# Optimization experiments

Hardware: AMD Instinct MI355X
Metric: run time of the kernel (lower is better)

## Reference

```python
import jax, jax.numpy as jnp
import numpy as np

I_DIM = 20000        # item (node) count; emb_mat has I_DIM+1 rows
EMB_DIM = 128        # input embedding dim
D_DIM = 128          # hidden (scaled) dim
N_EDGES = 640000     # number of (src, dst) edges


def setup_inputs() -> dict:
    key = jax.random.key(0)
    k1, k2, k3, k4 = jax.random.split(key, 4)
    emb_mat = jax.random.normal(k1, (I_DIM + 1, EMB_DIM), dtype=jnp.float32)
    # edges must be sorted by source node (column 0) so that the original
    # tf.repeat(segment_sums, bincount(src)) trick is well-defined.
    edge = jax.random.randint(k2, (N_EDGES, 2), 0, I_DIM + 1, dtype=jnp.int64)
    order = jnp.argsort(edge[:, 0])
    edge = edge[order]
    W_scale = jax.random.normal(k3, (EMB_DIM, D_DIM), dtype=jnp.float32) * 0.05
    b_scale = jnp.zeros((D_DIM,), dtype=jnp.float32)
    W_att = jax.random.normal(k4, (2 * D_DIM, 1), dtype=jnp.float32) * 0.05
    b_att = jnp.zeros((1,), dtype=jnp.float32)
    return {"emb_mat": emb_mat, "edge": edge, "W_scale": W_scale,
            "b_scale": b_scale, "W_att": W_att, "b_att": b_att}


def reference(emb_mat, edge, W_scale, b_scale, W_att, b_att):
    num_segments = emb_mat.shape[0]          # i_dim + 1
    seg = edge[:, 0]                         # source nodes (segment ids), [E]

    # gather both endpoints, scale: [E, 2, emb] -> [E, 2, d]
    edge_emb = emb_mat[edge] @ W_scale + b_scale
    E = edge_emb.shape[0]
    # attention logit per edge from concatenated endpoint features
    att = (edge_emb.reshape(E, -1) @ W_att + b_att)[:, 0]   # [E]
    att = jax.nn.leaky_relu(att, negative_slope=0.2)
    scores = jnp.exp(att - 1.0)                              # exp(att - ones)

    # manual segment softmax over edges grouped by source node
    score_sum = jax.ops.segment_sum(scores, seg, num_segments=num_segments)
    score_norm = scores / score_sum[seg]                     # [E]

    # scale all node embeddings once, gather destination features
    item_scaled = emb_mat @ W_scale + b_scale                # [N, d]
    items = item_scaled[edge[:, 1]]                          # [E, d]

    agg = jax.ops.segment_sum(score_norm[:, None] * items, seg,
                              num_segments=num_segments)     # [N, d]
    return jax.nn.sigmoid(agg)
```

## Files before the change

kernel.cpp:

```cpp
#include <hip/hip_runtime.h>
#include <math.h>

#define NSEG 20001
#define EMB  128
#define NE   640000

#define SCALE_BLOCKS 313
#define BOUNDS_BLOCKS 2500
#define APAD 136

typedef __attribute__((ext_vector_type(8))) short bf16x8;
typedef __attribute__((ext_vector_type(4))) float f32x4;

__device__ __forceinline__ unsigned f2bf(float x) {
    unsigned u = __float_as_uint(x);
    return (u + 0x7fffu + ((u >> 16) & 1u)) >> 16;
}
__device__ __forceinline__ float bfbits2f(unsigned h) { return __uint_as_float(h << 16); }

__global__ __launch_bounds__(256) void wconv_kernel(
    const float* __restrict__ W,
    unsigned short* __restrict__ wt_hi, unsigned short* __restrict__ wt_lo)
{
    const int c  = blockIdx.x * 8 + (threadIdx.x & 7);
    const int k0 = (threadIdx.x >> 3) * 4;
    unsigned h[4], l[4];
    #pragma unroll
    for (int i = 0; i < 4; ++i) {
        float x = W[(k0 + i) * EMB + c];
        h[i] = f2bf(x);
        l[i] = f2bf(x - bfbits2f(h[i]));
    }
    *(uint2*)&wt_hi[c * EMB + k0] = make_uint2(h[0] | (h[1] << 16), h[2] | (h[3] << 16));
    *(uint2*)&wt_lo[c * EMB + k0] = make_uint2(l[0] | (l[1] << 16), l[2] | (l[3] << 16));
}

__global__ __launch_bounds__(256) void prep_kernel(
    const float* __restrict__ emb,
    const unsigned short* __restrict__ wt_hi, const unsigned short* __restrict__ wt_lo,
    const float* __restrict__ bsc, const float* __restrict__ Watt,
    const int* __restrict__ edge,
    unsigned short* __restrict__ tab,
    float* __restrict__ a_src, float* __restrict__ a_dst,
    int* __restrict__ seg_start, int* __restrict__ dst)
{
    const int tid = threadIdx.x;
    if (blockIdx.x >= SCALE_BLOCKS) {
        int e = (blockIdx.x - SCALE_BLOCKS) * 256 + tid;
        int2 p = ((const int2*)edge)[e];
        dst[e] = p.y;
        int sp = __shfl_up(p.x, 1);
        if ((tid & 63) == 0) sp = (e == 0) ? -1 : edge[2*e - 2];
        for (int t = sp + 1; t <= p.x; ++t) seg_start[t] = e;
        if (e == NE - 1) {
            for (int t = p.x + 1; t <= NSEG; ++t) seg_start[t] = NE;
        }
        return;
    }

    __shared__ unsigned short Ah[64 * APAD];
    __shared__ unsigned short Al[64 * APAD];
    __shared__ float ps_part[4][64];
    __shared__ float pd_part[4][64];

    const int r0   = blockIdx.x * 64;
    const int w    = tid >> 6;
    const int lane = tid & 63;
    const int l15  = lane & 15;
    const int lk   = lane >> 4;

    const float4* embg4 = (const float4*)emb;
    const int gmax = NSEG * 32 - 1;
    #pragma unroll
    for (int j = 0; j < 8; ++j) {
        int idx = tid + j * 256;
        int row = idx >> 5, f4 = idx & 31;
        int g = r0 * 32 + idx;
        float4 v = embg4[g <= gmax ? g : gmax];
        unsigned h0 = f2bf(v.x), h1 = f2bf(v.y), h2 = f2bf(v.z), h3 = f2bf(v.w);
        unsigned l0 = f2bf(v.x - bfbits2f(h0)), l1 = f2bf(v.y - bfbits2f(h1));
        unsigned l2 = f2bf(v.z - bfbits2f(h2)), l3 = f2bf(v.w - bfbits2f(h3));
        int o = row * APAD + f4 * 4;
        *(uint2*)&Ah[o] = make_uint2(h0 | (h1 << 16), h2 | (h3 << 16));
        *(uint2*)&Al[o] = make_uint2(l0 | (l1 << 16), l2 | (l3 << 16));
    }
    __syncthreads();

    const int c0 = w * 16 + l15;
    const int c1 = c0 + 64;
    const bf16x8* Bh0p = (const bf16x8*)&wt_hi[c0 * EMB];
    const bf16x8* Bh1p = (const bf16x8*)&wt_hi[c1 * EMB];
    const bf16x8* Bl0p = (const bf16x8*)&wt_lo[c0 * EMB];
    const bf16x8* Bl1p = (const bf16x8*)&wt_lo[c1 * EMB];

    f32x4 acc[4][2];
    #pragma unroll
    for (int m = 0; m < 4; ++m) {
        acc[m][0] = (f32x4){0.f, 0.f, 0.f, 0.f};
        acc[m][1] = (f32x4){0.f, 0.f, 0.f, 0.f};
    }

    #pragma unroll
    for (int kt = 0; kt < 4; ++kt) {
        const int fo = kt * 4 + lk;
        bf16x8 Bh0 = Bh0p[fo], Bh1 = Bh1p[fo];
        bf16x8 Bl0 = Bl0p[fo], Bl1 = Bl1p[fo];
        #pragma unroll
        for (int m = 0; m < 4; ++m) {
            const int ao = (m * 16 + l15) * APAD + kt * 32 + lk * 8;
            bf16x8 Af = *(const bf16x8*)&Ah[ao];
            bf16x8 Lf = *(const bf16x8*)&Al[ao];
            acc[m][0] = __builtin_amdgcn_mfma_f32_16x16x32_bf16(Af, Bh0, acc[m][0], 0, 0, 0);
            acc[m][1] = __builtin_amdgcn_mfma_f32_16x16x32_bf16(Af, Bh1, acc[m][1], 0, 0, 0);
            acc[m][0] = __builtin_amdgcn_mfma_f32_16x16x32_bf16(Lf, Bh0, acc[m][0], 0, 0, 0);
            acc[m][1] = __builtin_amdgcn_mfma_f32_16x16x32_bf16(Lf, Bh1, acc[m][1], 0, 0, 0);
            acc[m][0] = __builtin_amdgcn_mfma_f32_16x16x32_bf16(Af, Bl0, acc[m][0], 0, 0, 0);
            acc[m][1] = __builtin_amdgcn_mfma_f32_16x16x32_bf16(Af, Bl1, acc[m][1], 0, 0, 0);
        }
    }

    const float bs0 = bsc[c0],        bs1 = bsc[c1];
    const float ws0 = Watt[c0],       ws1 = Watt[c1];
    const float wd0 = Watt[EMB + c0], wd1 = Watt[EMB + c1];

    #pragma unroll
    for (int m = 0; m < 4; ++m) {
        #pragma unroll
        for (int r = 0; r < 4; ++r) {
            float v0 = acc[m][0][r] + bs0;
            float v1 = acc[m][1][r] + bs1;
            const int rl  = m * 16 + lk * 4 + r;
            const int row = r0 + rl;
            if (row < NSEG)
                ((unsigned*)tab)[row * 64 + c0] = f2bf(v0) | (f2bf(v1) << 16);
            float ps = v0 * ws0 + v1 * ws1;
            float pd = v0 * wd0 + v1 * wd1;
            #pragma unroll
            for (int off = 8; off >= 1; off >>= 1) {
                ps += __shfl_xor(ps, off);
                pd += __shfl_xor(pd, off);
            }
            if (l15 == 0) { ps_part[w][rl] = ps; pd_part[w][rl] = pd; }
        }
    }
    __syncthreads();
    if (tid < 64) {
        const int row = r0 + tid;
        if (row < NSEG) {
            a_src[row] = ps_part[0][tid] + ps_part[1][tid] + ps_part[2][tid] + ps_part[3][tid];
            a_dst[row] = pd_part[0][tid] + pd_part[1][tid] + pd_part[2][tid] + pd_part[3][tid];
        }
    }
}

__device__ __forceinline__ float bf_lo(unsigned u) { return __uint_as_float(u << 16); }
__device__ __forceinline__ float bf_hi(unsigned u) { return __uint_as_float(u & 0xffff0000u); }
__device__ __forceinline__ float bcastf(float v, int j) {
    return __uint_as_float(__builtin_amdgcn_readlane(__float_as_uint(v), j));
}

__global__ __launch_bounds__(256) void agg_kernel(
    const int* __restrict__ dst, const float* __restrict__ a_src,
    const float* __restrict__ a_dst, const float* __restrict__ b_att,
    const int* __restrict__ seg_start, const unsigned int* __restrict__ tab32,
    float* __restrict__ out)
{
    const int wid = blockIdx.x * 4 + (threadIdx.x >> 6);
    if (wid >= NSEG) return;
    const int lane = threadIdx.x & 63;
    const unsigned int* tabl = tab32 + lane;

    const int s0 = seg_start[wid];
    const int s1 = seg_start[wid + 1];
    const float aS = a_src[wid] + b_att[0];

    float accx = 0.f, accy = 0.f, ssum = 0.f;

    for (int cb = s0; cb < s1; cb += 64) {
        int n = s1 - cb; if (n > 64) n = 64;
        int e = cb + lane;
        int dmine = 0; float sc = 0.f;
        if (lane < n) {
            dmine = dst[e] << 6;
            float att = aS + a_dst[dmine >> 6];
            att = att > 0.f ? att : 0.2f * att;
            sc  = expf(att - 1.f);
        }
        ssum += sc;

        int j = 0;
        for (; j + 7 < n; j += 8) {
            float w0 = bcastf(sc, j+0), w1 = bcastf(sc, j+1);
            float w2 = bcastf(sc, j+2), w3 = bcastf(sc, j+3);
            float w4 = bcastf(sc, j+4), w5 = bcastf(sc, j+5);
            float w6 = bcastf(sc, j+6), w7 = bcastf(sc, j+7);
            int d0 = __builtin_amdgcn_readlane(dmine, j+0);
            int d1 = __builtin_amdgcn_readlane(dmine, j+1);
            int d2 = __builtin_amdgcn_readlane(dmine, j+2);
            int d3 = __builtin_amdgcn_readlane(dmine, j+3);
            int d4 = __builtin_amdgcn_readlane(dmine, j+4);
            int d5 = __builtin_amdgcn_readlane(dmine, j+5);
            int d6 = __builtin_amdgcn_readlane(dmine, j+6);
            int d7 = __builtin_amdgcn_readlane(dmine, j+7);
            unsigned u0 = tabl[d0], u1 = tabl[d1], u2 = tabl[d2], u3 = tabl[d3];
            unsigned u4 = tabl[d4], u5 = tabl[d5], u6 = tabl[d6], u7 = tabl[d7];
            accx += w0 * bf_lo(u0); accy += w0 * bf_hi(u0);
            accx += w1 * bf_lo(u1); accy += w1 * bf_hi(u1);
            accx += w2 * bf_lo(u2); accy += w2 * bf_hi(u2);
            accx += w3 * bf_lo(u3); accy += w3 * bf_hi(u3);
            accx += w4 * bf_lo(u4); accy += w4 * bf_hi(u4);
            accx += w5 * bf_lo(u5); accy += w5 * bf_hi(u5);
            accx += w6 * bf_lo(u6); accy += w6 * bf_hi(u6);
            accx += w7 * bf_lo(u7); accy += w7 * bf_hi(u7);
        }
        for (; j < n; ++j) {
            float w = bcastf(sc, j);
            int   d = __builtin_amdgcn_readlane(dmine, j);
            unsigned u = tabl[d];
            accx += w * bf_lo(u);
            accy += w * bf_hi(u);
        }
    }

    #pragma unroll
    for (int off = 32; off >= 1; off >>= 1) ssum += __shfl_xor(ssum, off);

    const float inv = (s1 > s0) ? 1.f / ssum : 0.f;
    float ox = accx * inv, oy = accy * inv;
    ox = 1.f / (1.f + expf(-ox));
    oy = 1.f / (1.f + expf(-oy));
    out[wid * EMB + lane]      = ox;
    out[wid * EMB + 64 + lane] = oy;
}

extern "C" void kernel_launch(void* const* d_in, const int* in_sizes, int n_in,
                              void* d_out, int out_size, void* d_ws, size_t ws_size,
                              hipStream_t stream) {
    const float* emb  = (const float*)d_in[0];
    const int*   edge = (const int*)  d_in[1];
    const float* W    = (const float*)d_in[2];
    const float* bsc  = (const float*)d_in[3];
    const float* Watt = (const float*)d_in[4];
    const float* batt = (const float*)d_in[5];
    float* out = (float*)d_out;

    unsigned short* tab = (unsigned short*)d_ws;
    float* a_src = (float*)(tab + (size_t)NSEG * EMB);
    float* a_dst = a_src + NSEG;
    int*   seg_start = (int*)(a_dst + NSEG);
    int*   dstc = seg_start + NSEG + 3;
    unsigned short* wt_hi = (unsigned short*)((char*)d_ws + (32u << 20));
    unsigned short* wt_lo = wt_hi + EMB * EMB;

    wconv_kernel<<<16, 256, 0, stream>>>(W, wt_hi, wt_lo);
    prep_kernel<<<SCALE_BLOCKS + BOUNDS_BLOCKS, 256, 0, stream>>>(
        emb, wt_hi, wt_lo, bsc, Watt, edge, tab, a_src, a_dst, seg_start, dstc);
    agg_kernel<<<(NSEG + 3) / 4, 256, 0, stream>>>(
        dstc, a_src, a_dst, batt, seg_start, (const unsigned int*)tab, out);
}
```

Baseline: 107.6 us.

## Fuse weight bf16 split into prep kernel and use hardware packed bf16 convert

```diff
diff --git a/kernel.cpp b/kernel.cpp
--- a/kernel.cpp
+++ b/kernel.cpp
@@ -12,32 +12,22 @@
 typedef __attribute__((ext_vector_type(8))) short bf16x8;
 typedef __attribute__((ext_vector_type(4))) float f32x4;
 
-__device__ __forceinline__ unsigned f2bf(float x) {
-    unsigned u = __float_as_uint(x);
-    return (u + 0x7fffu + ((u >> 16) & 1u)) >> 16;
-}
-__device__ __forceinline__ float bfbits2f(unsigned h) { return __uint_as_float(h << 16); }
-
-__global__ __launch_bounds__(256) void wconv_kernel(
-    const float* __restrict__ W,
-    unsigned short* __restrict__ wt_hi, unsigned short* __restrict__ wt_lo)
-{
-    const int c  = blockIdx.x * 8 + (threadIdx.x & 7);
-    const int k0 = (threadIdx.x >> 3) * 4;
-    unsigned h[4], l[4];
-    #pragma unroll
-    for (int i = 0; i < 4; ++i) {
-        float x = W[(k0 + i) * EMB + c];
-        h[i] = f2bf(x);
-        l[i] = f2bf(x - bfbits2f(h[i]));
-    }
-    *(uint2*)&wt_hi[c * EMB + k0] = make_uint2(h[0] | (h[1] << 16), h[2] | (h[3] << 16));
-    *(uint2*)&wt_lo[c * EMB + k0] = make_uint2(l[0] | (l[1] << 16), l[2] | (l[3] << 16));
+__device__ __forceinline__ unsigned cvt_pk_bf16(float lo, float hi) {
+    unsigned r;
+    asm("v_cvt_pk_bf16_f32 %0, %1, %2" : "=v"(r) : "v"(lo), "v"(hi));
+    return r;
+}
+__device__ __forceinline__ float bfbits2f_lo(unsigned p) { return __uint_as_float(p << 16); }
+__device__ __forceinline__ float bfbits2f_hi(unsigned p) { return __uint_as_float(p & 0xffff0000u); }
+
+__device__ __forceinline__ bf16x8 pack4(unsigned a, unsigned b, unsigned c, unsigned d) {
+    union { unsigned u[4]; bf16x8 v; } t;
+    t.u[0] = a; t.u[1] = b; t.u[2] = c; t.u[3] = d;
+    return t.v;
 }
 
 __global__ __launch_bounds__(256) void prep_kernel(
-    const float* __restrict__ emb,
-    const unsigned short* __restrict__ wt_hi, const unsigned short* __restrict__ wt_lo,
+    const float* __restrict__ emb, const float* __restrict__ W,
     const float* __restrict__ bsc, const float* __restrict__ Watt,
     const int* __restrict__ edge,
     unsigned short* __restrict__ tab,
@@ -77,21 +67,20 @@
         int row = idx >> 5, f4 = idx & 31;
         int g = r0 * 32 + idx;
         float4 v = embg4[g <= gmax ? g : gmax];
-        unsigned h0 = f2bf(v.x), h1 = f2bf(v.y), h2 = f2bf(v.z), h3 = f2bf(v.w);
-        unsigned l0 = f2bf(v.x - bfbits2f(h0)), l1 = f2bf(v.y - bfbits2f(h1));
-        unsigned l2 = f2bf(v.z - bfbits2f(h2)), l3 = f2bf(v.w - bfbits2f(h3));
+        unsigned h01 = cvt_pk_bf16(v.x, v.y);
+        unsigned h23 = cvt_pk_bf16(v.z, v.w);
+        unsigned l01 = cvt_pk_bf16(v.x - bfbits2f_lo(h01), v.y - bfbits2f_hi(h01));
+        unsigned l23 = cvt_pk_bf16(v.z - bfbits2f_lo(h23), v.w - bfbits2f_hi(h23));
         int o = row * APAD + f4 * 4;
-        *(uint2*)&Ah[o] = make_uint2(h0 | (h1 << 16), h2 | (h3 << 16));
-        *(uint2*)&Al[o] = make_uint2(l0 | (l1 << 16), l2 | (l3 << 16));
+        *(uint2*)&Ah[o] = make_uint2(h01, h23);
+        *(uint2*)&Al[o] = make_uint2(l01, l23);
     }
     __syncthreads();
 
     const int c0 = w * 16 + l15;
     const int c1 = c0 + 64;
-    const bf16x8* Bh0p = (const bf16x8*)&wt_hi[c0 * EMB];
-    const bf16x8* Bh1p = (const bf16x8*)&wt_hi[c1 * EMB];
-    const bf16x8* Bl0p = (const bf16x8*)&wt_lo[c0 * EMB];
-    const bf16x8* Bl1p = (const bf16x8*)&wt_lo[c1 * EMB];
+    const float* Wc0 = W + c0;
+    const float* Wc1 = W + c1;
 
     f32x4 acc[4][2];
     #pragma unroll
@@ -102,9 +91,27 @@
 
     #pragma unroll
     for (int kt = 0; kt < 4; ++kt) {
-        const int fo = kt * 4 + lk;
-        bf16x8 Bh0 = Bh0p[fo], Bh1 = Bh1p[fo];
-        bf16x8 Bl0 = Bl0p[fo], Bl1 = Bl1p[fo];
+        const int kb = kt * 32 + lk * 8;
+        float x0[8], x1[8];
+        #pragma unroll
+        for (int i = 0; i < 8; ++i) {
+            x0[i] = Wc0[(kb + i) * EMB];
+            x1[i] = Wc1[(kb + i) * EMB];
+        }
+        unsigned bh0[4], bl0[4], bh1[4], bl1[4];
+        #pragma unroll
+        for (int i = 0; i < 4; ++i) {
+            unsigned h0 = cvt_pk_bf16(x0[2*i], x0[2*i+1]);
+            unsigned h1 = cvt_pk_bf16(x1[2*i], x1[2*i+1]);
+            bl0[i] = cvt_pk_bf16(x0[2*i] - bfbits2f_lo(h0), x0[2*i+1] - bfbits2f_hi(h0));
+            bl1[i] = cvt_pk_bf16(x1[2*i] - bfbits2f_lo(h1), x1[2*i+1] - bfbits2f_hi(h1));
+            bh0[i] = h0; bh1[i] = h1;
+        }
+        bf16x8 Bh0 = pack4(bh0[0], bh0[1], bh0[2], bh0[3]);
+        bf16x8 Bh1 = pack4(bh1[0], bh1[1], bh1[2], bh1[3]);
+        bf16x8 Bl0 = pack4(bl0[0], bl0[1], bl0[2], bl0[3]);
+        bf16x8 Bl1 = pack4(bl1[0], bl1[1], bl1[2], bl1[3]);
+
         #pragma unroll
         for (int m = 0; m < 4; ++m) {
             const int ao = (m * 16 + l15) * APAD + kt * 32 + lk * 8;
@@ -132,7 +139,7 @@
             const int rl  = m * 16 + lk * 4 + r;
             const int row = r0 + rl;
             if (row < NSEG)
-                ((unsigned*)tab)[row * 64 + c0] = f2bf(v0) | (f2bf(v1) << 16);
+                ((unsigned*)tab)[row * 64 + c0] = cvt_pk_bf16(v0, v1);
             float ps = v0 * ws0 + v1 * ws1;
             float pd = v0 * wd0 + v1 * wd1;
             #pragma unroll
@@ -249,12 +256,9 @@
     float* a_dst = a_src + NSEG;
     int*   seg_start = (int*)(a_dst + NSEG);
     int*   dstc = seg_start + NSEG + 3;
-    unsigned short* wt_hi = (unsigned short*)((char*)d_ws + (32u << 20));
-    unsigned short* wt_lo = wt_hi + EMB * EMB;
-
-    wconv_kernel<<<16, 256, 0, stream>>>(W, wt_hi, wt_lo);
+
     prep_kernel<<<SCALE_BLOCKS + BOUNDS_BLOCKS, 256, 0, stream>>>(
-        emb, wt_hi, wt_lo, bsc, Watt, edge, tab, a_src, a_dst, seg_start, dstc);
+        emb, W, bsc, Watt, edge, tab, a_src, a_dst, seg_start, dstc);
     agg_kernel<<<(NSEG + 3) / 4, 256, 0, stream>>>(
         dstc, a_src, a_dst, batt, seg_start, (const unsigned int*)tab, out);
 }
```

Result: faster. 102.4 us (-4.8%).
